# Kernel optimization log

Hardware: AMD Instinct MI355X
Metric: run time of the kernel (lower is better)

Reference implementation:

```python
import jax, jax.numpy as jnp
import numpy as np

HIGHEST_ID = 222.0
ZERO_NONZERO_PENALTY = 1.0
N_COEFFS = 447  # Chebyshev.fit(..., deg=446)


def _cheb_eval(x, coeffs):
    """Evaluate sum_i coeffs[i] * T_i(x/111 - 1) via O(1)-memory three-term recurrence."""
    xn = x / 111.0 - 1.0
    T0 = jnp.ones_like(xn)
    T1 = xn
    acc0 = coeffs[0] * T0 + coeffs[1] * T1

    def step(carry, c):
        Tm1, Tn, acc = carry
        Tnew = 2.0 * xn * Tn - Tm1
        acc = acc + c * Tnew
        return (Tn, Tnew, acc), None

    (_, _, acc), _ = jax.lax.scan(step, (T0, T1, acc0), coeffs[2:])
    return acc


def _round_ste(x):
    return x + jax.lax.stop_gradient(jnp.round(x) - x)


def _mask(x):
    # ~0 for id > 222, ~id for id <= 222
    return x * jax.nn.sigmoid(50.0 * (222.5 - x))


def setup_inputs() -> dict:
    key = jax.random.key(0)
    k0, k1, k2 = jax.random.split(key, 3)
    shape = (512, 7, 16, 64, 2)
    scale = jnp.array([222.0, 200.0], dtype=jnp.float32)  # (id, amount)
    y_pred = jax.random.uniform(k0, shape, dtype=jnp.float32) * scale
    y = jax.random.uniform(k1, shape, dtype=jnp.float32) * scale
    calories_coeffs = jax.random.normal(k2, (N_COEFFS,), dtype=jnp.float32) * 0.1
    return {"y_pred": y_pred, "y": y, "calories_coeffs": calories_coeffs}


def reference(y_pred, y, calories_coeffs):
    pred_ids = y_pred[..., 0]
    pred_amounts = y_pred[..., 1]
    true_ids = y[..., 0]
    true_amounts = y[..., 1]

    id_zero_mask = 1.0 - jnp.tanh(4.0 * pred_ids)
    amount_nonzero_mask = jnp.tanh(4.0 * pred_amounts)
    case1 = id_zero_mask * amount_nonzero_mask
    case2 = (1.0 - id_zero_mask) * (1.0 - amount_nonzero_mask)
    zeros_nonzeros_penalty = (ZERO_NONZERO_PENALTY * (case1 + case2)).sum(axis=(1, 2, 3)).mean()

    id_range_penalty = jax.nn.relu(pred_ids - HIGHEST_ID).sum(axis=(1, 2, 3)).mean()

    B = y.shape[0]
    true_amounts_f = true_amounts.reshape(B, -1)
    true_calories = _cheb_eval(true_ids, calories_coeffs).reshape(B, -1)
    calories_in_true_menu = (true_calories * true_amounts_f / 100.0).sum(axis=1) / 7.0

    pred_amounts_f = pred_amounts.reshape(y_pred.shape[0], -1)
    pred_calories = _cheb_eval(_mask(_round_ste(pred_ids)), calories_coeffs).reshape(y_pred.shape[0], -1)
    calories_in_pred_menu = (pred_calories * pred_amounts_f / 100.0).sum(axis=1) / 7.0

    calories_diff = ((calories_in_true_menu - calories_in_pred_menu) ** 2).mean()

    return zeros_nonzeros_penalty + id_range_penalty + calories_diff
```

## Files before the change

### kernel.cpp

```cpp
#include <hip/hip_runtime.h>
#include <cmath>


constexpr int NCOEF = 447;
constexpr int NTAB  = 223;
constexpr int M     = 65536;
constexpr float H_STEP = (float)(3.14159265358979323846 / 65536.0);
constexpr float SCALE  = (float)(65536.0 / 3.14159265358979323846);
constexpr int SLICES = 7;
constexpr int TPB = 256;

__device__ float2 g_tab[M];
__device__ float  g_pred[NTAB];
__device__ float4 g_part[512 * SLICES];

__device__ __forceinline__ float tanh4(float v) {
  float e = __expf(8.0f * v);
  return fmaf(-2.0f, __builtin_amdgcn_rcpf(e + 1.0f), 1.0f);
}

__global__ __launch_bounds__(256)
void build_tables(const float* __restrict__ coeffs)
{
  int g = blockIdx.x * 256 + threadIdx.x;
  float x;
  if (g <= M) {
    x = cosf((float)g * H_STEP);
  } else if (g < M + 1 + NTAB) {
    float kf = (float)(g - (M + 1));
    float m = kf / (1.0f + __expf(50.0f * (kf - 222.5f)));
    x = m / 111.0f - 1.0f;
  } else {
    return;
  }
  float x2 = x + x;
  float Ta = 1.0f, Tb = x;
  float acc = fmaf(coeffs[1], x, coeffs[0]);
  for (int i = 2; i + 1 < NCOEF; i += 2) {
    Ta = fmaf(x2, Tb, -Ta); acc = fmaf(coeffs[i],     Ta, acc);
    Tb = fmaf(x2, Ta, -Tb); acc = fmaf(coeffs[i + 1], Tb, acc);
  }
  Ta = fmaf(x2, Tb, -Ta); acc = fmaf(coeffs[NCOEF - 1], Ta, acc);

  if (g <= M) {
    if (g < M) g_tab[g].x = acc;
    if (g > 0) g_tab[g - 1].y = acc;
  } else {
    g_pred[g - (M + 1)] = acc;
  }
}

__global__ __launch_bounds__(TPB)
void loss_main(const float2* __restrict__ yp, const float2* __restrict__ yt)
{
  __shared__ float spred[NTAB];
  __shared__ float sred[12];
  const int tid = threadIdx.x;

  if (tid < NTAB) spred[tid] = g_pred[tid];
  __syncthreads();

  const size_t base = (size_t)blockIdx.y * 7168 + (size_t)blockIdx.x * 1024;
  const float2* P = yp + base;
  const float2* T = yt + base;

  float pen = 0.0f, cp = 0.0f, ct = 0.0f;

  #pragma unroll
  for (int k = 0; k < 4; ++k) {
    float2 pv = P[tid + k * TPB];
    float2 tv = T[tid + k * TPB];

    float a = tanh4(pv.x);
    float bb = tanh4(pv.y);
    pen += fmaf(bb, fmaf(-2.0f, a, 1.0f), a) + fmaxf(pv.x - 222.0f, 0.0f);

    int idx = (int)rintf(pv.x);
    idx = idx < 0 ? 0 : (idx > NTAB - 1 ? NTAB - 1 : idx);
    cp = fmaf(spred[idx], pv.y, cp);

    float xn = tv.x / 111.0f - 1.0f;
    float t = acosf(xn) * SCALE;
    int i = (int)t;
    i = i > M - 1 ? M - 1 : i;
    float fr = t - (float)i;
    float2 f2 = g_tab[i];
    float cal = fmaf(fr, f2.y - f2.x, f2.x);
    ct = fmaf(cal, tv.y, ct);
  }

  #pragma unroll
  for (int o = 32; o > 0; o >>= 1) {
    pen += __shfl_down(pen, o, 64);
    ct  += __shfl_down(ct,  o, 64);
    cp  += __shfl_down(cp,  o, 64);
  }
  const int w = tid >> 6;
  if ((tid & 63) == 0) { sred[w] = pen; sred[4 + w] = ct; sred[8 + w] = cp; }
  __syncthreads();
  if (tid == 0) {
    g_part[blockIdx.y * SLICES + blockIdx.x] =
        make_float4(sred[0] + sred[1] + sred[2]  + sred[3],
                    sred[4] + sred[5] + sred[6]  + sred[7],
                    sred[8] + sred[9] + sred[10] + sred[11], 0.0f);
  }
}

__global__ __launch_bounds__(512)
void finalize(float* __restrict__ out)
{
  __shared__ float sr[8];
  int t = threadIdx.x;
  float pen = 0.0f, ct = 0.0f, cp = 0.0f;
  #pragma unroll
  for (int s = 0; s < SLICES; ++s) {
    float4 p = g_part[t * SLICES + s];
    pen += p.x; ct += p.y; cp += p.z;
  }
  float d = (ct - cp) * (1.0f / 700.0f);
  float v = fmaf(d, d, pen);
  #pragma unroll
  for (int o = 32; o > 0; o >>= 1) v += __shfl_down(v, o, 64);
  if ((t & 63) == 0) sr[t >> 6] = v;
  __syncthreads();
  if (t == 0) {
    out[0] = (sr[0] + sr[1] + sr[2] + sr[3] +
              sr[4] + sr[5] + sr[6] + sr[7]) * (1.0f / 512.0f);
  }
}

extern "C" void kernel_launch(void* const* d_in, const int* in_sizes, int n_in,
                              void* d_out, int out_size, void* d_ws, size_t ws_size,
                              hipStream_t stream) {
  build_tables<<<257, 256, 0, stream>>>((const float*)d_in[2]);
  loss_main<<<dim3(SLICES, 512), TPB, 0, stream>>>(
      (const float2*)d_in[0], (const float2*)d_in[1]);
  finalize<<<1, 512, 0, stream>>>((float*)d_out);
}
```

Measured before the change: 114.1 us.

## Use float4 loads, split each batch into two blocks, batch loads ahead of compute

The main loss kernel now reads inputs as float4, so each load carries two (id, amount) pairs. The grid changes from 7x512 blocks of 1024 elements to 1024 blocks that each cover half a batch row of 3584 elements. All seven loads per thread are issued up front, then all 14 table gathers, then the arithmetic, to raise memory-level parallelism and hide gather latency. The cost is higher register pressure from the held arrays, and the finalize kernel is adjusted to combine two partials per batch.

```diff
diff --git a/kernel.cpp b/kernel.cpp
--- a/kernel.cpp
+++ b/kernel.cpp
@@ -7,12 +7,12 @@
 constexpr int M     = 65536;
 constexpr float H_STEP = (float)(3.14159265358979323846 / 65536.0);
 constexpr float SCALE  = (float)(65536.0 / 3.14159265358979323846);
-constexpr int SLICES = 7;
 constexpr int TPB = 256;
+constexpr int F4_PER_HALF = 1792;
 
 __device__ float2 g_tab[M];
 __device__ float  g_pred[NTAB];
-__device__ float4 g_part[512 * SLICES];
+__device__ float4 g_part[1024];
 
 __device__ __forceinline__ float tanh4(float v) {
   float e = __expf(8.0f * v);
@@ -51,7 +51,7 @@
 }
 
 __global__ __launch_bounds__(TPB)
-void loss_main(const float2* __restrict__ yp, const float2* __restrict__ yt)
+void loss_main(const float4* __restrict__ yp4, const float4* __restrict__ yt4)
 {
   __shared__ float spred[NTAB];
   __shared__ float sred[12];
@@ -60,33 +60,52 @@
   if (tid < NTAB) spred[tid] = g_pred[tid];
   __syncthreads();
 
-  const size_t base = (size_t)blockIdx.y * 7168 + (size_t)blockIdx.x * 1024;
-  const float2* P = yp + base;
-  const float2* T = yt + base;
+  const int b = blockIdx.x >> 1, h = blockIdx.x & 1;
+  const size_t base = (size_t)b * 3584 + (size_t)h * F4_PER_HALF;
 
-  float pen = 0.0f, cp = 0.0f, ct = 0.0f;
+  float4 p[7], t[7];
+  #pragma unroll
+  for (int k = 0; k < 7; ++k) {
+    p[k] = yp4[base + tid + k * TPB];
+    t[k] = yt4[base + tid + k * TPB];
+  }
 
+  float fr[14], tam[14];
+  float2 f2[14];
   #pragma unroll
-  for (int k = 0; k < 4; ++k) {
-    float2 pv = P[tid + k * TPB];
-    float2 tv = T[tid + k * TPB];
+  for (int k = 0; k < 7; ++k) {
+    float xn0 = t[k].x / 111.0f - 1.0f;
+    float th0 = acosf(xn0) * SCALE;
+    int i0 = (int)th0; i0 = i0 > M - 1 ? M - 1 : i0;
+    fr[2 * k] = th0 - (float)i0; tam[2 * k] = t[k].y;
+    f2[2 * k] = g_tab[i0];
 
-    float a = tanh4(pv.x);
-    float bb = tanh4(pv.y);
-    pen += fmaf(bb, fmaf(-2.0f, a, 1.0f), a) + fmaxf(pv.x - 222.0f, 0.0f);
+    float xn1 = t[k].z / 111.0f - 1.0f;
+    float th1 = acosf(xn1) * SCALE;
+    int i1 = (int)th1; i1 = i1 > M - 1 ? M - 1 : i1;
+    fr[2 * k + 1] = th1 - (float)i1; tam[2 * k + 1] = t[k].w;
+    f2[2 * k + 1] = g_tab[i1];
+  }
 
-    int idx = (int)rintf(pv.x);
-    idx = idx < 0 ? 0 : (idx > NTAB - 1 ? NTAB - 1 : idx);
-    cp = fmaf(spred[idx], pv.y, cp);
+  float ct = 0.0f;
+  #pragma unroll
+  for (int k = 0; k < 14; ++k) {
+    float cal = fmaf(fr[k], f2[k].y - f2[k].x, f2[k].x);
+    ct = fmaf(cal, tam[k], ct);
+  }
 
-    float xn = tv.x / 111.0f - 1.0f;
-    float t = acosf(xn) * SCALE;
-    int i = (int)t;
-    i = i > M - 1 ? M - 1 : i;
-    float fr = t - (float)i;
-    float2 f2 = g_tab[i];
-    float cal = fmaf(fr, f2.y - f2.x, f2.x);
-    ct = fmaf(cal, tv.y, ct);
+  float pen = 0.0f, cp = 0.0f;
+  #pragma unroll
+  for (int k = 0; k < 7; ++k) {
+    float id0 = p[k].x, am0 = p[k].y, id1 = p[k].z, am1 = p[k].w;
+    float a0 = tanh4(id0), b0 = tanh4(am0);
+    pen += fmaf(b0, fmaf(-2.0f, a0, 1.0f), a0) + fmaxf(id0 - 222.0f, 0.0f);
+    int x0 = (int)rintf(id0); x0 = x0 < 0 ? 0 : (x0 > NTAB - 1 ? NTAB - 1 : x0);
+    cp = fmaf(spred[x0], am0, cp);
+    float a1 = tanh4(id1), b1 = tanh4(am1);
+    pen += fmaf(b1, fmaf(-2.0f, a1, 1.0f), a1) + fmaxf(id1 - 222.0f, 0.0f);
+    int x1 = (int)rintf(id1); x1 = x1 < 0 ? 0 : (x1 > NTAB - 1 ? NTAB - 1 : x1);
+    cp = fmaf(spred[x1], am1, cp);
   }
 
   #pragma unroll
@@ -99,7 +118,7 @@
   if ((tid & 63) == 0) { sred[w] = pen; sred[4 + w] = ct; sred[8 + w] = cp; }
   __syncthreads();
   if (tid == 0) {
-    g_part[blockIdx.y * SLICES + blockIdx.x] =
+    g_part[blockIdx.x] =
         make_float4(sred[0] + sred[1] + sred[2]  + sred[3],
                     sred[4] + sred[5] + sred[6]  + sred[7],
                     sred[8] + sred[9] + sred[10] + sred[11], 0.0f);
@@ -111,17 +130,13 @@
 {
   __shared__ float sr[8];
   int t = threadIdx.x;
-  float pen = 0.0f, ct = 0.0f, cp = 0.0f;
+  float4 u = g_part[2 * t], v = g_part[2 * t + 1];
+  float pen = u.x + v.x;
+  float d = ((u.y + v.y) - (u.z + v.z)) * (1.0f / 700.0f);
+  float s = fmaf(d, d, pen);
   #pragma unroll
-  for (int s = 0; s < SLICES; ++s) {
-    float4 p = g_part[t * SLICES + s];
-    pen += p.x; ct += p.y; cp += p.z;
-  }
-  float d = (ct - cp) * (1.0f / 700.0f);
-  float v = fmaf(d, d, pen);
-  #pragma unroll
-  for (int o = 32; o > 0; o >>= 1) v += __shfl_down(v, o, 64);
-  if ((t & 63) == 0) sr[t >> 6] = v;
+  for (int o = 32; o > 0; o >>= 1) s += __shfl_down(s, o, 64);
+  if ((t & 63) == 0) sr[t >> 6] = s;
   __syncthreads();
   if (t == 0) {
     out[0] = (sr[0] + sr[1] + sr[2] + sr[3] +
@@ -133,7 +148,7 @@
                               void* d_out, int out_size, void* d_ws, size_t ws_size,
                               hipStream_t stream) {
   build_tables<<<257, 256, 0, stream>>>((const float*)d_in[2]);
-  loss_main<<<dim3(SLICES, 512), TPB, 0, stream>>>(
-      (const float2*)d_in[0], (const float2*)d_in[1]);
+  loss_main<<<1024, TPB, 0, stream>>>(
+      (const float4*)d_in[0], (const float4*)d_in[1]);
   finalize<<<1, 512, 0, stream>>>((float*)d_out);
 }
```

Result: slower. 116.8 us (+2.3%).
